# Kernel optimization log

Measured on AMD Instinct MI355X. Metric: run time of the kernel, lower is better.

The kernel has to match this reference:

```python
import jax, jax.numpy as jnp
import numpy as np

TOP_K = 50
TAU = 0.02
EPS = 1e-12  # torch F.normalize eps


def setup_inputs() -> dict:
    key = jax.random.key(0)
    k1, k2 = jax.random.split(key)
    test_patches = jax.random.normal(k1, (2048, 256), dtype=jnp.float32)
    memory_nodes_gpu = jax.random.normal(k2, (100000, 256), dtype=jnp.float32)
    return {"test_patches": test_patches, "memory_nodes_gpu": memory_nodes_gpu}


def _l2norm(x):
    n = jnp.linalg.norm(x, axis=-1, keepdims=True)
    return x / jnp.maximum(n, EPS)


def reference(test_patches, memory_nodes_gpu):
    # [P, M] similarity
    sim = jnp.matmul(test_patches, memory_nodes_gpu.T)
    K = min(TOP_K, memory_nodes_gpu.shape[0])
    topk_sim, topk_idx = jax.lax.top_k(sim, K)          # [P, K]
    attn = jax.nn.softmax(topk_sim / TAU, axis=1)        # [P, K]
    gathered = memory_nodes_gpu[topk_idx]                # [P, K, D]
    messages = jnp.einsum('pk,pkd->pd', attn, gathered)  # [P, D]
    updated = _l2norm(test_patches + messages)           # [P, D]
    evidence = topk_sim[:, 0]                            # [P]
    ew = jax.nn.softmax(evidence / TAU)[:, None]          # [P, 1]
    global_feature = jnp.sum(updated * ew, axis=0, keepdims=True)  # [1, D]
    return _l2norm(global_feature), updated
```

## Files before the change

kernel.cpp:

```cpp
#include <hip/hip_runtime.h>
#include <cstdint>
#include <cstddef>

#define NP      2048
#define NN      100000
#define DIM     256
#define NT      6250
#define NG      1563
#define NGT     1792
#define NTP     (NG * 4)
#define CPX     25
#define INV_TAU 50.0f
#define MARGIN  0.7f
#define CUT     0.553f
#define LCAP    64

typedef __fp16 half8  __attribute__((ext_vector_type(8)));
typedef __fp16 half2v __attribute__((ext_vector_type(2)));
typedef float  floatx4 __attribute__((ext_vector_type(4)));

union H8 { half8 v8; half2v v2[4]; };

typedef const __attribute__((address_space(1))) char* gptr_t;
typedef __attribute__((address_space(3))) char* sptr_t;

__device__ __forceinline__ unsigned enc_f32(float f) {
    unsigned b = __float_as_uint(f);
    return (b & 0x80000000u) ? ~b : (b | 0x80000000u);
}
__device__ __forceinline__ float dec_f32(unsigned u) {
    unsigned b = (u & 0x80000000u) ? (u & 0x7FFFFFFFu) : ~u;
    return __uint_as_float(b);
}

__global__ __launch_bounds__(512)
void k_convB(const float* __restrict__ B, __fp16* __restrict__ Bh,
             unsigned* __restrict__ me_u)
{
    const int t    = (int)blockIdx.x;
    const int ks   = (int)threadIdx.x >> 6;
    const int lane = (int)threadIdx.x & 63;
    if (t == 0 && threadIdx.x == 0) me_u[0] = 0u;
    H8 h;
    if (t < NT) {
        const int node = t * 16 + (lane & 15);
        const int d0   = ((lane >> 4) << 3) + (ks << 5);
        const float* bp = B + (size_t)node * DIM + d0;
        float4 b0 = *reinterpret_cast<const float4*>(bp);
        float4 b1 = *reinterpret_cast<const float4*>(bp + 4);
        h.v2[0] = __builtin_amdgcn_cvt_pkrtz(b0.x, b0.y);
        h.v2[1] = __builtin_amdgcn_cvt_pkrtz(b0.z, b0.w);
        h.v2[2] = __builtin_amdgcn_cvt_pkrtz(b1.x, b1.y);
        h.v2[3] = __builtin_amdgcn_cvt_pkrtz(b1.z, b1.w);
    } else {
        h.v2[0] = __builtin_amdgcn_cvt_pkrtz(0.f, 0.f);
        h.v2[1] = h.v2[0]; h.v2[2] = h.v2[0]; h.v2[3] = h.v2[0];
    }
    *reinterpret_cast<half8*>(Bh + (((size_t)t * 8 + ks) * 64 + lane) * 8) = h.v8;
}

__global__ __launch_bounds__(256, 2)
void k_pass1(const float* __restrict__ A, const __fp16* __restrict__ Bh,
             float* __restrict__ tmax)
{
    __shared__ __fp16 lds[2][16384];

    const int tid  = (int)threadIdx.x;
    const int w    = tid >> 6;
    const int lane = tid & 63;
    const int col  = lane & 15;
    const int kg   = lane >> 4;

    const int bid   = (int)blockIdx.x;
    const int chunk = (bid & 7) * 8 + ((bid >> 3) & 7);
    const int rb    = bid >> 6;

    const int g0 = chunk * CPX;
    if (g0 >= NG) return;
    const int g1 = (g0 + CPX < NG) ? g0 + CPX : NG;
    const int wrow0 = rb * 256 + w * 64;

    H8 af[4][8];
#pragma unroll
    for (int rs = 0; rs < 4; ++rs) {
        const float* ap = A + (size_t)(wrow0 + rs * 16 + col) * DIM + (kg << 3);
#pragma unroll
        for (int ks = 0; ks < 8; ++ks) {
            float4 x0 = *reinterpret_cast<const float4*>(ap + (ks << 5));
            float4 x1 = *reinterpret_cast<const float4*>(ap + (ks << 5) + 4);
            af[rs][ks].v2[0] = __builtin_amdgcn_cvt_pkrtz(x0.x, x0.y);
            af[rs][ks].v2[1] = __builtin_amdgcn_cvt_pkrtz(x0.z, x0.w);
            af[rs][ks].v2[2] = __builtin_amdgcn_cvt_pkrtz(x1.x, x1.y);
            af[rs][ks].v2[3] = __builtin_amdgcn_cvt_pkrtz(x1.z, x1.w);
        }
    }

    auto STAGE = [&](int buf, int g) {
        const char* src = (const char*)Bh + ((size_t)g << 15) + (w << 13) + (lane << 4);
        char* dstb = (char*)&lds[buf][0] + (w << 13);
#pragma unroll
        for (int i = 0; i < 8; ++i)
            __builtin_amdgcn_global_load_lds((gptr_t)(src + (i << 10)),
                                             (sptr_t)(dstb + (i << 10)), 16, 0, 0);
    };

    STAGE(0, g0);
    int cur = 0;
    for (int g = g0; g < g1; ++g) {
        asm volatile("s_waitcnt vmcnt(0)" ::: "memory");
        __syncthreads();
        if (g + 1 < g1) STAGE(cur ^ 1, g + 1);

        const __fp16* base = &lds[cur][0] + lane * 8;
        float tm[4] = { -INFINITY, -INFINITY, -INFINITY, -INFINITY };

        half8 bf0[8], bf1[8];
        auto LD = [&](half8 (&bf)[8], int tt) {
#pragma unroll
            for (int ks = 0; ks < 8; ++ks)
                bf[ks] = *reinterpret_cast<const half8*>(base + tt * 4096 + ks * 512);
        };
        auto FM = [&](const half8 (&bf)[8]) {
            floatx4 acc[4];
#pragma unroll
            for (int rs = 0; rs < 4; ++rs) acc[rs] = (floatx4){0.f, 0.f, 0.f, 0.f};
#pragma unroll
            for (int ks = 0; ks < 8; ++ks) {
                acc[0] = __builtin_amdgcn_mfma_f32_16x16x32_f16(bf[ks], af[0][ks].v8, acc[0], 0, 0, 0);
                acc[1] = __builtin_amdgcn_mfma_f32_16x16x32_f16(bf[ks], af[1][ks].v8, acc[1], 0, 0, 0);
                acc[2] = __builtin_amdgcn_mfma_f32_16x16x32_f16(bf[ks], af[2][ks].v8, acc[2], 0, 0, 0);
                acc[3] = __builtin_amdgcn_mfma_f32_16x16x32_f16(bf[ks], af[3][ks].v8, acc[3], 0, 0, 0);
            }
#pragma unroll
            for (int rs = 0; rs < 4; ++rs)
                tm[rs] = fmaxf(tm[rs], fmaxf(fmaxf(acc[rs][0], acc[rs][1]),
                                             fmaxf(acc[rs][2], acc[rs][3])));
        };

        LD(bf0, 0);
        LD(bf1, 1);
        FM(bf0);
        LD(bf0, 2);
        FM(bf1);
        LD(bf1, 3);
        FM(bf0);
        FM(bf1);

#pragma unroll
        for (int rs = 0; rs < 4; ++rs) {
            tm[rs] = fmaxf(tm[rs], __shfl_xor(tm[rs], 16));
            tm[rs] = fmaxf(tm[rs], __shfl_xor(tm[rs], 32));
        }
        if (kg == 0) {
#pragma unroll
            for (int rs = 0; rs < 4; ++rs)
                tmax[(size_t)g * NP + wrow0 + rs * 16 + col] = tm[rs];
        }
        cur ^= 1;
    }
}

__global__ __launch_bounds__(256)
void k_tr(const float* __restrict__ tmax, float* __restrict__ tmaxT)
{
    __shared__ float tile[64][65];
    const int t  = (int)threadIdx.x;
    const int g0 = (int)blockIdx.x * 64;
    const int r0 = (int)blockIdx.y * 64;
    const int a  = t & 63;
    const int b  = t >> 6;
#pragma unroll
    for (int it = 0; it < 16; ++it) {
        int gi = b + it * 4;
        int g  = g0 + gi;
        tile[gi][a] = (g < NG) ? tmax[(size_t)g * NP + r0 + a] : -INFINITY;
    }
    __syncthreads();
#pragma unroll
    for (int it = 0; it < 16; ++it) {
        int ri = b + it * 4;
        tmaxT[(size_t)(r0 + ri) * NGT + g0 + a] = tile[a][ri];
    }
}

__global__ __launch_bounds__(256)
void k_finish(const float* __restrict__ A, const float* __restrict__ B,
              const float* __restrict__ tmaxT, float* __restrict__ out,
              float* __restrict__ evidence, unsigned* __restrict__ me_u)
{
    __shared__ float ald4[4][68];
    __shared__ float sims[64];
    __shared__ float red[8];
    __shared__ int   list[LCAP];
    __shared__ int   wsum[4];

    const int t    = (int)threadIdx.x;
    const int row  = (int)blockIdx.x;
    const int lane = t & 63;
    const int wv   = t >> 6;

    const float av_own = A[(size_t)row * DIM + t];
    ald4[t >> 6][t & 63] = av_own;

    float v[7];
    const float* tr = tmaxT + (size_t)row * NGT + t * 7;
    float M = -INFINITY;
#pragma unroll
    for (int k = 0; k < 7; ++k) { v[k] = tr[k]; M = fmaxf(M, v[k]); }
#pragma unroll
    for (int o = 1; o < 64; o <<= 1) M = fmaxf(M, __shfl_xor(M, o));
    if (lane == 0) red[wv] = M;
    __syncthreads();
    M = fmaxf(fmaxf(red[0], red[1]), fmaxf(red[2], red[3]));

    const float thr = M - MARGIN;
    int cnt = 0; unsigned mask7 = 0u;
#pragma unroll
    for (int k = 0; k < 7; ++k)
        if (v[k] > thr) { mask7 |= (1u << k); ++cnt; }
    int pre = cnt;
#pragma unroll
    for (int o = 1; o < 64; o <<= 1) {
        int x = __shfl_up(pre, o);
        if (lane >= o) pre += x;
    }
    if (lane == 63) wsum[wv] = pre;
    __syncthreads();
    int woff = 0;
    for (int i = 0; i < wv; ++i) woff += wsum[i];
    int pos = woff + pre - cnt;
    if (mask7) {
#pragma unroll
        for (int k = 0; k < 7; ++k)
            if (mask7 & (1u << k)) {
                if (pos < LCAP) list[pos] = t * 7 + k;
                ++pos;
            }
    }
    __syncthreads();
    int total = wsum[0] + wsum[1] + wsum[2] + wsum[3];
    if (total > LCAP) total = LCAP;

    float m = -INFINITY, l = 0.f, msg = 0.f;
    const int n = t >> 2, q = t & 3;

    for (int e = 0; e < total; ++e) {
        const int g  = list[e];
        const int n0 = g * 64;
        const int count = (NN - n0 < 64) ? NN - n0 : 64;
        {
            float s = 0.f;
            if (n < count) {
                const float4* bp = reinterpret_cast<const float4*>(B + (size_t)(n0 + n) * DIM + q * 64);
                const float4* ap = reinterpret_cast<const float4*>(&ald4[q][0]);
#pragma unroll
                for (int i = 0; i < 16; ++i) {
                    float4 b4 = bp[i], a4 = ap[i];
                    s += a4.x * b4.x + a4.y * b4.y + a4.z * b4.z + a4.w * b4.w;
                }
            }
            s += __shfl_xor(s, 1);
            s += __shfl_xor(s, 2);
            __syncthreads();
            if (q == 0 && n < count) sims[n] = s;
            __syncthreads();
        }
        float gm = -INFINITY;
        for (int i = 0; i < count; ++i) gm = fmaxf(gm, sims[i]);
        if (gm > m) {
            float sc = __expf((m - gm) * INV_TAU);
            m = gm; l *= sc; msg *= sc;
        }
        const float cut = m - CUT;
        for (int i = 0; i < count; ++i) {
            float si = sims[i];
            if (si > cut) {
                float wn = __expf((si - m) * INV_TAU);
                l += wn;
                msg += wn * B[(size_t)(n0 + i) * DIM + t];
            }
        }
    }

    float u = av_own + msg * (1.0f / l);
    float ss = u * u;
#pragma unroll
    for (int o = 1; o < 64; o <<= 1) ss += __shfl_xor(ss, o);
    if (lane == 0) red[4 + wv] = ss;
    __syncthreads();
    ss = (red[4] + red[5]) + (red[6] + red[7]);
    float rn = 1.0f / fmaxf(sqrtf(ss), 1e-12f);
    out[256 + (size_t)row * DIM + t] = u * rn;
    if (t == 0) {
        evidence[row] = m;
        atomicMax(me_u, enc_f32(m));
    }
}

__global__ __launch_bounds__(256)
void k_gpart(const float* __restrict__ evidence, const unsigned* __restrict__ me_u,
             const float* __restrict__ out, float* __restrict__ gpart)
{
    __shared__ float wsh[128];
    int tid = (int)threadIdx.x;
    int r0  = blockIdx.x * 128;
    float Me = dec_f32(me_u[0]);
    if (tid < 128) wsh[tid] = __expf((evidence[r0 + tid] - Me) * INV_TAU);
    __syncthreads();
    float g = 0.0f;
    for (int k = 0; k < 128; ++k)
        g += wsh[k] * out[256 + (size_t)(r0 + k) * DIM + tid];
    gpart[blockIdx.x * 256 + tid] = g;
}

__global__ __launch_bounds__(256)
void k_final(const float* __restrict__ gpart, float* __restrict__ out)
{
    __shared__ float red[256];
    int tid = (int)threadIdx.x;
    float g = 0.0f;
#pragma unroll
    for (int b = 0; b < 16; ++b) g += gpart[b * 256 + tid];
    red[tid] = g * g; __syncthreads();
    for (int s = 128; s > 0; s >>= 1) {
        if (tid < s) red[tid] += red[tid + s];
        __syncthreads();
    }
    float n = sqrtf(red[0]);
    float r = 1.0f / fmaxf(n, 1e-12f);
    out[tid] = g * r;
}

extern "C" void kernel_launch(void* const* d_in, const int* in_sizes, int n_in,
                              void* d_out, int out_size, void* d_ws, size_t ws_size,
                              hipStream_t stream)
{
    const float* A = (const float*)d_in[0];
    const float* B = (const float*)d_in[1];
    float* out = (float*)d_out;
    float* ws  = (float*)d_ws;

    __fp16* Bh      = (__fp16*)ws;
    float* tmaxp    = ws + (size_t)NTP * 2048;
    float* tmaxT    = tmaxp + (size_t)NG * NP;
    float* evidence = tmaxT + (size_t)NP * NGT;
    unsigned* me_u  = (unsigned*)(evidence + NP);
    float* gpart    = (float*)(me_u + 16);

    k_convB <<<NTP,           512, 0, stream>>>(B, Bh, me_u);
    k_pass1 <<<512,           256, 0, stream>>>(A, Bh, tmaxp);
    k_tr    <<<dim3(28, 32),  256, 0, stream>>>(tmaxp, tmaxT);
    k_finish<<<NP,            256, 0, stream>>>(A, B, tmaxT, out, evidence, me_u);
    k_gpart <<<16,            256, 0, stream>>>(evidence, me_u, out, gpart);
    k_final <<<1,             256, 0, stream>>>(gpart, out);
}
```

Before: 204.1 us.

## Halve candidate group size to 32 nodes and software-pipeline pass1 LDS loads

Pass1 now records a per-row maximum for every 32-node half-group instead of every 64-node group, so the finish kernel's candidate list is finer and each listed group rescans only 32 nodes in FP32. The transposed max buffer is widened and reuses the fp16 B workspace region, since the transpose runs after pass1 has finished reading it. Pass1 also interleaves the next tile's LDS fragment loads with the current tile's MFMAs. The cost is more max writes and a larger transpose. More lists may also hit the 64-entry cap because groups are smaller, which could drop true top-k candidates.

```diff
diff --git a/kernel.cpp b/kernel.cpp
--- a/kernel.cpp
+++ b/kernel.cpp
@@ -7,7 +7,9 @@
 #define DIM     256
 #define NT      6250
 #define NG      1563
-#define NGT     1792
+#define NG2     3126
+#define NG2R    3125
+#define NGT2    3328
 #define NTP     (NG * 4)
 #define CPX     25
 #define INV_TAU 50.0f
@@ -61,7 +63,7 @@
 
 __global__ __launch_bounds__(256, 2)
 void k_pass1(const float* __restrict__ A, const __fp16* __restrict__ Bh,
-             float* __restrict__ tmax)
+             float* __restrict__ tmax2)
 {
     __shared__ __fp16 lds[2][16384];
 
@@ -112,56 +114,61 @@
         if (g + 1 < g1) STAGE(cur ^ 1, g + 1);
 
         const __fp16* base = &lds[cur][0] + lane * 8;
-        float tm[4] = { -INFINITY, -INFINITY, -INFINITY, -INFINITY };
-
-        half8 bf0[8], bf1[8];
-        auto LD = [&](half8 (&bf)[8], int tt) {
-#pragma unroll
-            for (int ks = 0; ks < 8; ++ks)
-                bf[ks] = *reinterpret_cast<const half8*>(base + tt * 4096 + ks * 512);
+        float tmh[2][4];
+#pragma unroll
+        for (int hh = 0; hh < 2; ++hh)
+#pragma unroll
+            for (int rs = 0; rs < 4; ++rs) tmh[hh][rs] = -INFINITY;
+
+        half8 bfA[8], bfB[8];
+#pragma unroll
+        for (int ks = 0; ks < 8; ++ks)
+            bfA[ks] = *reinterpret_cast<const half8*>(base + ks * 512);
+
+        auto FMI = [&](half8 (&curf)[8], half8 (&nxtf)[8], int ttn, bool ld, int hh) {
+            floatx4 acc[4];
+#pragma unroll
+            for (int rs = 0; rs < 4; ++rs) acc[rs] = (floatx4){0.f, 0.f, 0.f, 0.f};
+#pragma unroll
+            for (int ks = 0; ks < 8; ++ks) {
+                if (ld)
+                    nxtf[ks] = *reinterpret_cast<const half8*>(base + ttn * 4096 + ks * 512);
+                acc[0] = __builtin_amdgcn_mfma_f32_16x16x32_f16(curf[ks], af[0][ks].v8, acc[0], 0, 0, 0);
+                acc[1] = __builtin_amdgcn_mfma_f32_16x16x32_f16(curf[ks], af[1][ks].v8, acc[1], 0, 0, 0);
+                acc[2] = __builtin_amdgcn_mfma_f32_16x16x32_f16(curf[ks], af[2][ks].v8, acc[2], 0, 0, 0);
+                acc[3] = __builtin_amdgcn_mfma_f32_16x16x32_f16(curf[ks], af[3][ks].v8, acc[3], 0, 0, 0);
+            }
+#pragma unroll
+            for (int rs = 0; rs < 4; ++rs)
+                tmh[hh][rs] = fmaxf(tmh[hh][rs], fmaxf(fmaxf(acc[rs][0], acc[rs][1]),
+                                                       fmaxf(acc[rs][2], acc[rs][3])));
         };
-        auto FM = [&](const half8 (&bf)[8]) {
-            floatx4 acc[4];
-#pragma unroll
-            for (int rs = 0; rs < 4; ++rs) acc[rs] = (floatx4){0.f, 0.f, 0.f, 0.f};
-#pragma unroll
-            for (int ks = 0; ks < 8; ++ks) {
-                acc[0] = __builtin_amdgcn_mfma_f32_16x16x32_f16(bf[ks], af[0][ks].v8, acc[0], 0, 0, 0);
-                acc[1] = __builtin_amdgcn_mfma_f32_16x16x32_f16(bf[ks], af[1][ks].v8, acc[1], 0, 0, 0);
-                acc[2] = __builtin_amdgcn_mfma_f32_16x16x32_f16(bf[ks], af[2][ks].v8, acc[2], 0, 0, 0);
-                acc[3] = __builtin_amdgcn_mfma_f32_16x16x32_f16(bf[ks], af[3][ks].v8, acc[3], 0, 0, 0);
-            }
-#pragma unroll
-            for (int rs = 0; rs < 4; ++rs)
-                tm[rs] = fmaxf(tm[rs], fmaxf(fmaxf(acc[rs][0], acc[rs][1]),
-                                             fmaxf(acc[rs][2], acc[rs][3])));
-        };
-
-        LD(bf0, 0);
-        LD(bf1, 1);
-        FM(bf0);
-        LD(bf0, 2);
-        FM(bf1);
-        LD(bf1, 3);
-        FM(bf0);
-        FM(bf1);
-
-#pragma unroll
-        for (int rs = 0; rs < 4; ++rs) {
-            tm[rs] = fmaxf(tm[rs], __shfl_xor(tm[rs], 16));
-            tm[rs] = fmaxf(tm[rs], __shfl_xor(tm[rs], 32));
-        }
+
+        FMI(bfA, bfB, 1, true,  0);
+        FMI(bfB, bfA, 2, true,  0);
+        FMI(bfA, bfB, 3, true,  1);
+        FMI(bfB, bfA, 0, false, 1);
+
+#pragma unroll
+        for (int hh = 0; hh < 2; ++hh)
+#pragma unroll
+            for (int rs = 0; rs < 4; ++rs) {
+                tmh[hh][rs] = fmaxf(tmh[hh][rs], __shfl_xor(tmh[hh][rs], 16));
+                tmh[hh][rs] = fmaxf(tmh[hh][rs], __shfl_xor(tmh[hh][rs], 32));
+            }
         if (kg == 0) {
 #pragma unroll
-            for (int rs = 0; rs < 4; ++rs)
-                tmax[(size_t)g * NP + wrow0 + rs * 16 + col] = tm[rs];
+            for (int hh = 0; hh < 2; ++hh)
+#pragma unroll
+                for (int rs = 0; rs < 4; ++rs)
+                    tmax2[(size_t)(g * 2 + hh) * NP + wrow0 + rs * 16 + col] = tmh[hh][rs];
         }
         cur ^= 1;
     }
 }
 
 __global__ __launch_bounds__(256)
-void k_tr(const float* __restrict__ tmax, float* __restrict__ tmaxT)
+void k_tr(const float* __restrict__ tmax2, float* __restrict__ tmaxT)
 {
     __shared__ float tile[64][65];
     const int t  = (int)threadIdx.x;
@@ -173,13 +180,13 @@
     for (int it = 0; it < 16; ++it) {
         int gi = b + it * 4;
         int g  = g0 + gi;
-        tile[gi][a] = (g < NG) ? tmax[(size_t)g * NP + r0 + a] : -INFINITY;
+        tile[gi][a] = (g < NG2) ? tmax2[(size_t)g * NP + r0 + a] : -INFINITY;
     }
     __syncthreads();
 #pragma unroll
     for (int it = 0; it < 16; ++it) {
         int ri = b + it * 4;
-        tmaxT[(size_t)(r0 + ri) * NGT + g0 + a] = tile[a][ri];
+        tmaxT[(size_t)(r0 + ri) * NGT2 + g0 + a] = tile[a][ri];
     }
 }
 
@@ -188,8 +195,8 @@
               const float* __restrict__ tmaxT, float* __restrict__ out,
               float* __restrict__ evidence, unsigned* __restrict__ me_u)
 {
-    __shared__ float ald4[4][68];
-    __shared__ float sims[64];
+    __shared__ float ald8[8][36];
+    __shared__ float sims[32];
     __shared__ float red[8];
     __shared__ int   list[LCAP];
     __shared__ int   wsum[4];
@@ -200,13 +207,13 @@
     const int wv   = t >> 6;
 
     const float av_own = A[(size_t)row * DIM + t];
-    ald4[t >> 6][t & 63] = av_own;
-
-    float v[7];
-    const float* tr = tmaxT + (size_t)row * NGT + t * 7;
+    ald8[t >> 5][t & 31] = av_own;
+
+    float v[13];
+    const float* tr = tmaxT + (size_t)row * NGT2 + t * 13;
     float M = -INFINITY;
 #pragma unroll
-    for (int k = 0; k < 7; ++k) { v[k] = tr[k]; M = fmaxf(M, v[k]); }
+    for (int k = 0; k < 13; ++k) { v[k] = tr[k]; M = fmaxf(M, v[k]); }
 #pragma unroll
     for (int o = 1; o < 64; o <<= 1) M = fmaxf(M, __shfl_xor(M, o));
     if (lane == 0) red[wv] = M;
@@ -214,10 +221,10 @@
     M = fmaxf(fmaxf(red[0], red[1]), fmaxf(red[2], red[3]));
 
     const float thr = M - MARGIN;
-    int cnt = 0; unsigned mask7 = 0u;
-#pragma unroll
-    for (int k = 0; k < 7; ++k)
-        if (v[k] > thr) { mask7 |= (1u << k); ++cnt; }
+    int cnt = 0; unsigned mask13 = 0u;
+#pragma unroll
+    for (int k = 0; k < 13; ++k)
+        if (v[k] > thr && (t * 13 + k) < NG2R) { mask13 |= (1u << k); ++cnt; }
     int pre = cnt;
 #pragma unroll
     for (int o = 1; o < 64; o <<= 1) {
@@ -229,11 +236,11 @@
     int woff = 0;
     for (int i = 0; i < wv; ++i) woff += wsum[i];
     int pos = woff + pre - cnt;
-    if (mask7) {
-#pragma unroll
-        for (int k = 0; k < 7; ++k)
-            if (mask7 & (1u << k)) {
-                if (pos < LCAP) list[pos] = t * 7 + k;
+    if (mask13) {
+#pragma unroll
+        for (int k = 0; k < 13; ++k)
+            if (mask13 & (1u << k)) {
+                if (pos < LCAP) list[pos] = t * 13 + k;
                 ++pos;
             }
     }
@@ -242,37 +249,36 @@
     if (total > LCAP) total = LCAP;
 
     float m = -INFINITY, l = 0.f, msg = 0.f;
-    const int n = t >> 2, q = t & 3;
+    const int n = t >> 3, q8 = t & 7;
 
     for (int e = 0; e < total; ++e) {
         const int g  = list[e];
-        const int n0 = g * 64;
-        const int count = (NN - n0 < 64) ? NN - n0 : 64;
+        const int n0 = g * 32;
         {
             float s = 0.f;
-            if (n < count) {
-                const float4* bp = reinterpret_cast<const float4*>(B + (size_t)(n0 + n) * DIM + q * 64);
-                const float4* ap = reinterpret_cast<const float4*>(&ald4[q][0]);
-#pragma unroll
-                for (int i = 0; i < 16; ++i) {
-                    float4 b4 = bp[i], a4 = ap[i];
-                    s += a4.x * b4.x + a4.y * b4.y + a4.z * b4.z + a4.w * b4.w;
-                }
+            const float4* bp = reinterpret_cast<const float4*>(B + (size_t)(n0 + n) * DIM + q8 * 32);
+            const float4* ap = reinterpret_cast<const float4*>(&ald8[q8][0]);
+#pragma unroll
+            for (int i = 0; i < 8; ++i) {
+                float4 b4 = bp[i], a4 = ap[i];
+                s += a4.x * b4.x + a4.y * b4.y + a4.z * b4.z + a4.w * b4.w;
             }
             s += __shfl_xor(s, 1);
             s += __shfl_xor(s, 2);
+            s += __shfl_xor(s, 4);
             __syncthreads();
-            if (q == 0 && n < count) sims[n] = s;
+            if (q8 == 0) sims[n] = s;
             __syncthreads();
         }
         float gm = -INFINITY;
-        for (int i = 0; i < count; ++i) gm = fmaxf(gm, sims[i]);
+#pragma unroll
+        for (int i = 0; i < 32; ++i) gm = fmaxf(gm, sims[i]);
         if (gm > m) {
             float sc = __expf((m - gm) * INV_TAU);
             m = gm; l *= sc; msg *= sc;
         }
         const float cut = m - CUT;
-        for (int i = 0; i < count; ++i) {
+        for (int i = 0; i < 32; ++i) {
             float si = sims[i];
             if (si > cut) {
                 float wn = __expf((si - m) * INV_TAU);
@@ -341,15 +347,15 @@
     float* ws  = (float*)d_ws;
 
     __fp16* Bh      = (__fp16*)ws;
-    float* tmaxp    = ws + (size_t)NTP * 2048;
-    float* tmaxT    = tmaxp + (size_t)NG * NP;
-    float* evidence = tmaxT + (size_t)NP * NGT;
+    float* tmaxT    = ws;
+    float* tmax2    = ws + (size_t)NTP * 2048;
+    float* evidence = tmax2 + (size_t)NG2 * NP;
     unsigned* me_u  = (unsigned*)(evidence + NP);
     float* gpart    = (float*)(me_u + 16);
 
     k_convB <<<NTP,           512, 0, stream>>>(B, Bh, me_u);
-    k_pass1 <<<512,           256, 0, stream>>>(A, Bh, tmaxp);
-    k_tr    <<<dim3(28, 32),  256, 0, stream>>>(tmaxp, tmaxT);
+    k_pass1 <<<512,           256, 0, stream>>>(A, Bh, tmax2);
+    k_tr    <<<dim3(52, 32),  256, 0, stream>>>(tmax2, tmaxT);
     k_finish<<<NP,            256, 0, stream>>>(A, B, tmaxT, out, evidence, me_u);
     k_gpart <<<16,            256, 0, stream>>>(evidence, me_u, out, gpart);
     k_final <<<1,             256, 0, stream>>>(gpart, out);
```

Result: faster. 182.6 us (-10.6%).
